# Performance work log

Measured on AMD Instinct MI355X. Metric: run time of the kernel, lower is better.

Reference implementation:

```python
import jax, jax.numpy as jnp
import numpy as np

B, T, E, H = 2, 2048, 2048, 16
D = E // H


def setup_inputs() -> dict:
    key = jax.random.key(0)
    ks = jax.random.split(key, 5)
    s = 0.02
    return {
        "x": jax.random.normal(ks[0], (B, T, E), jnp.float32),
        "Wq": jax.random.normal(ks[1], (E, E), jnp.float32) * s,
        "Wk": jax.random.normal(ks[2], (E, E), jnp.float32) * s,
        "Wv": jax.random.normal(ks[3], (E, E), jnp.float32) * s,
        "Wp": jax.random.normal(ks[4], (E, E), jnp.float32) * s,
        "bp": jnp.zeros((E,), jnp.float32),
    }


def reference(x, Wq, Wk, Wv, Wp, bp):
    b, t, e = x.shape
    h, d = H, E // H
    # torch Linear: y = x @ W.T (no bias for qkv)
    Q = (x @ Wq.T).reshape(b, h, t, d)  # faithful: view without transpose
    K = (x @ Wk.T).reshape(b, h, t, d)
    V = (x @ Wv.T).reshape(b, h, t, d)
    scores = jnp.einsum("bhqd,bhkd->bhqk", Q, K)
    causal = jnp.triu(jnp.ones((t, t), bool), k=1)  # True above diagonal
    scores = jnp.where(causal, -jnp.inf, scores)
    weights = jax.nn.softmax(scores / jnp.sqrt(jnp.float32(d)), axis=-1)
    # dropout p=0.0 (eval) -> identity
    ctx = jnp.einsum("bhqk,bhkd->bhqd", weights, V)  # (b,h,t,d)
    ctx = ctx.transpose(0, 2, 1, 3).reshape(b, t, e)
    return ctx @ Wp.T + bp
```

## Files before the change

### kernel.cpp

```cpp
#include <hip/hip_runtime.h>

#define SEQ   2048
#define EMB   2048
#define NHEAD 16
#define HDIM  128
#define ROWSM 4096

typedef float  f32x4   __attribute__((ext_vector_type(4)));
typedef float  f32x16  __attribute__((ext_vector_type(16)));
typedef __bf16 bf16x8  __attribute__((ext_vector_type(8)));

__device__ __forceinline__ unsigned short f2bf(float f) {
  union { __bf16 b; unsigned short u; } v; v.b = (__bf16)f; return v.u;
}
__device__ __forceinline__ unsigned int pk2(float a, float b) {
  return (unsigned int)f2bf(a) | ((unsigned int)f2bf(b) << 16);
}
__device__ __forceinline__ float max3f(float a, float b, float c) {
  return fmaxf(fmaxf(a, b), c);
}

__device__ __forceinline__ void gload16(const void* g, void* l) {
  __builtin_amdgcn_global_load_lds(
      (__attribute__((address_space(1))) const unsigned int*)g,
      (__attribute__((address_space(3))) unsigned int*)l,
      16, 0, 0);
}

__global__ void cvt_bf16(const float* __restrict__ in,
                         unsigned short* __restrict__ out, int n4) {
  int i = blockIdx.x * 256 + threadIdx.x;
  if (i >= n4) return;
  float4 v = ((const float4*)in)[i];
  ushort4 o;
  o.x = f2bf(v.x); o.y = f2bf(v.y); o.z = f2bf(v.z); o.w = f2bf(v.w);
  ((ushort4*)out)[i] = o;
}

__global__ void cvt_bf16_3(const float* __restrict__ i0, const float* __restrict__ i1,
                           const float* __restrict__ i2, unsigned short* __restrict__ o,
                           int n4) {
  const float* in = (blockIdx.z == 0) ? i0 : (blockIdx.z == 1) ? i1 : i2;
  unsigned short* out = o + (size_t)blockIdx.z * EMB * EMB;
  int i = blockIdx.x * 256 + threadIdx.x;
  if (i >= n4) return;
  float4 v = ((const float4*)in)[i];
  ushort4 o4;
  o4.x = f2bf(v.x); o4.y = f2bf(v.y); o4.z = f2bf(v.z); o4.w = f2bf(v.w);
  ((ushort4*)out)[i] = o4;
}

__global__ __launch_bounds__(512, 1) void gemm192_qkv(
    const unsigned short* __restrict__ A, const unsigned short* __restrict__ B,
    unsigned short* __restrict__ Cb) {
  __shared__ __align__(16) unsigned short At[2][256 * 64];
  __shared__ __align__(16) unsigned short Bt[2][192 * 64];

  const int tid  = threadIdx.x;
  const int lane = tid & 63;
  const int w    = tid >> 6;
  const int wr   = w >> 2;
  const int wc   = w & 3;
  const int lg   = lane >> 4;
  const int lc   = lane & 15;

  const int bid = blockIdx.x;
  const int xcd = bid & 7;
  const int j   = bid >> 3;
  const int mt  = xcd * 2 + (j >> 5);
  const int nt  = j & 31;
  const int m0 = mt * 256;
  const int n0 = nt * 192;

  const int srow8 = lane >> 3;
  const int sslot = (lane & 7) ^ srow8;
  const int NT = EMB / 64;

  auto stageAeven = [&](int ts) {
    if (ts >= NT) return;
    int buf = ts & 1, k0 = ts * 64;
    { int c = w;      int row = c * 8 + srow8;
      gload16(A + (size_t)(m0 + row) * EMB + k0 + sslot * 8, (char*)&At[buf][0] + c * 1024); }
    { int c = 16 + w; int row = c * 8 + srow8;
      gload16(A + (size_t)(m0 + row) * EMB + k0 + sslot * 8, (char*)&At[buf][0] + c * 1024); }
  };
  auto stageAodd = [&](int ts) {
    if (ts >= NT) return;
    int buf = ts & 1, k0 = ts * 64;
    { int c = 8 + w;  int row = c * 8 + srow8;
      gload16(A + (size_t)(m0 + row) * EMB + k0 + sslot * 8, (char*)&At[buf][0] + c * 1024); }
    { int c = 24 + w; int row = c * 8 + srow8;
      gload16(A + (size_t)(m0 + row) * EMB + k0 + sslot * 8, (char*)&At[buf][0] + c * 1024); }
  };
  auto stageB = [&](int ts) {
    if (ts >= NT) return;
    int buf = ts & 1, k0 = ts * 64;
#pragma unroll
    for (int s = 0; s < 3; ++s) {
      int c = w + s * 8;
      int row = c * 8 + srow8;
      gload16(B + (size_t)(n0 + row) * EMB + k0 + sslot * 8, (char*)&Bt[buf][0] + c * 1024);
    }
  };

  f32x4 acc[8][3] = {};
  bf16x8 afr[4][2], bfr[3][2];

  stageAeven(0); stageB(0); stageAodd(0); stageAeven(1); stageB(1);
  asm volatile("s_waitcnt vmcnt(7)" ::: "memory");
  __builtin_amdgcn_s_barrier();

  for (int t = 0; t < NT; ++t) {
    const char* ab = (const char*)&At[t & 1][0];
    const char* bb = (const char*)&Bt[t & 1][0];

#pragma unroll
    for (int ni = 0; ni < 3; ++ni)
#pragma unroll
      for (int kk = 0; kk < 2; ++kk) {
        int row = wc * 48 + ni * 16 + lc;
        bfr[ni][kk] = *(const bf16x8*)(bb + row * 128 + ((((kk << 2) | lg) ^ (lc & 7)) << 4));
      }
#pragma unroll
    for (int mi = 0; mi < 4; ++mi)
#pragma unroll
      for (int kk = 0; kk < 2; ++kk) {
        int row = wr * 128 + mi * 16 + lc;
        afr[mi][kk] = *(const bf16x8*)(ab + row * 128 + ((((kk << 2) | lg) ^ (lc & 7)) << 4));
      }
    stageAodd(t + 1);
    __builtin_amdgcn_s_barrier();
    asm volatile("s_waitcnt lgkmcnt(0)" ::: "memory");
    __builtin_amdgcn_sched_barrier(0);
    __builtin_amdgcn_s_setprio(1);
#pragma unroll
    for (int mi = 0; mi < 4; ++mi)
#pragma unroll
      for (int ni = 0; ni < 3; ++ni)
#pragma unroll
        for (int kk = 0; kk < 2; ++kk)
          acc[mi][ni] = __builtin_amdgcn_mfma_f32_16x16x32_bf16(
              afr[mi][kk], bfr[ni][kk], acc[mi][ni], 0, 0, 0);
    __builtin_amdgcn_s_setprio(0);
    if (t + 1 < NT) asm volatile("s_waitcnt vmcnt(7)" ::: "memory");
    else            asm volatile("s_waitcnt vmcnt(0)" ::: "memory");
    __builtin_amdgcn_s_barrier();

#pragma unroll
    for (int mi = 0; mi < 4; ++mi)
#pragma unroll
      for (int kk = 0; kk < 2; ++kk) {
        int row = wr * 128 + 64 + mi * 16 + lc;
        afr[mi][kk] = *(const bf16x8*)(ab + row * 128 + ((((kk << 2) | lg) ^ (lc & 7)) << 4));
      }
    stageAeven(t + 2); stageB(t + 2);
    __builtin_amdgcn_s_barrier();
    asm volatile("s_waitcnt lgkmcnt(0)" ::: "memory");
    __builtin_amdgcn_sched_barrier(0);
    __builtin_amdgcn_s_setprio(1);
#pragma unroll
    for (int mi = 0; mi < 4; ++mi)
#pragma unroll
      for (int ni = 0; ni < 3; ++ni)
#pragma unroll
        for (int kk = 0; kk < 2; ++kk)
          acc[4 + mi][ni] = __builtin_amdgcn_mfma_f32_16x16x32_bf16(
              afr[mi][kk], bfr[ni][kk], acc[4 + mi][ni], 0, 0, 0);
    __builtin_amdgcn_s_setprio(0);
    if (t + 2 < NT)      asm volatile("s_waitcnt vmcnt(7)" ::: "memory");
    else if (t + 1 < NT) asm volatile("s_waitcnt vmcnt(2)" ::: "memory");
    __builtin_amdgcn_s_barrier();
  }

#pragma unroll
  for (int mi = 0; mi < 8; ++mi)
#pragma unroll
    for (int ni = 0; ni < 3; ++ni) {
      int col = n0 + wc * 48 + ni * 16 + lc;
      unsigned short* dst = Cb + (size_t)(col >> 11) * ROWSM * EMB + (col & 2047);
#pragma unroll
      for (int rr = 0; rr < 4; ++rr) {
        int row = m0 + wr * 128 + mi * 16 + lg * 4 + rr;
        dst[(size_t)row * EMB] = f2bf(acc[mi][ni][rr]);
      }
    }
}

__global__ __launch_bounds__(512, 1) void gemm_p8(
    const unsigned short* __restrict__ A, const unsigned short* __restrict__ B,
    float* __restrict__ Cout, const float* __restrict__ bias) {
  __shared__ __align__(16) unsigned short At[2][128 * 64];
  __shared__ __align__(16) unsigned short Bt[2][256 * 64];

  const int tid  = threadIdx.x;
  const int lane = tid & 63;
  const int w    = tid >> 6;
  const int wr   = w >> 2;
  const int wc   = w & 3;
  const int lg   = lane >> 4;
  const int lc   = lane & 15;

  const int bid = blockIdx.x;
  const int xcd = bid & 7;
  const int j   = bid >> 3;
  const int mt  = xcd * 4 + (j >> 3);
  const int nt  = j & 7;
  const int m0 = mt * 128;
  const int n0 = nt * 256;

  const int srow8 = lane >> 3;
  const int sslot = (lane & 7) ^ srow8;
  const int NT = EMB / 64;

  auto stageA = [&](int ts) {
    if (ts >= NT) return;
    int buf = ts & 1, k0 = ts * 64;
#pragma unroll
    for (int rr = 0; rr < 2; ++rr) {
      int c = w + rr * 8;
      int row = c * 8 + srow8;
      gload16(A + (size_t)(m0 + row) * EMB + k0 + sslot * 8, (char*)&At[buf][0] + c * 1024);
    }
  };
  auto stageBlow = [&](int ts) {
    if (ts >= NT) return;
    int buf = ts & 1, k0 = ts * 64;
#pragma unroll
    for (int rr = 0; rr < 2; ++rr) {
      int i = w + rr * 8;
      int c = (i >> 2) * 8 + (i & 3);
      int row = c * 8 + srow8;
      gload16(B + (size_t)(n0 + row) * EMB + k0 + sslot * 8, (char*)&Bt[buf][0] + c * 1024);
    }
  };
  auto stageBhigh = [&](int ts) {
    if (ts >= NT) return;
    int buf = ts & 1, k0 = ts * 64;
#pragma unroll
    for (int rr = 0; rr < 2; ++rr) {
      int i = w + rr * 8;
      int c = (i >> 2) * 8 + 4 + (i & 3);
      int row = c * 8 + srow8;
      gload16(B + (size_t)(n0 + row) * EMB + k0 + sslot * 8, (char*)&Bt[buf][0] + c * 1024);
    }
  };

  f32x4 acc[4][4] = {};
  bf16x8 afr[4][2], bfr0[2][2], bfr1[2][2];

  stageA(0); stageBlow(0); stageBhigh(0); stageA(1); stageBlow(1);
  asm volatile("s_waitcnt vmcnt(6)" ::: "memory");
  __builtin_amdgcn_s_barrier();

  for (int t = 0; t < NT; ++t) {
    const char* ab = (const char*)&At[t & 1][0];
    const char* bb = (const char*)&Bt[t & 1][0];

#pragma unroll
    for (int ni = 0; ni < 2; ++ni)
#pragma unroll
      for (int kk = 0; kk < 2; ++kk) {
        int row = wc * 64 + ni * 16 + lc;
        bfr0[ni][kk] = *(const bf16x8*)(bb + row * 128 + ((((kk << 2) | lg) ^ (lc & 7)) << 4));
      }
#pragma unroll
    for (int mi = 0; mi < 4; ++mi)
#pragma unroll
      for (int kk = 0; kk < 2; ++kk) {
        int row = wr * 64 + mi * 16 + lc;
        afr[mi][kk] = *(const bf16x8*)(ab + row * 128 + ((((kk << 2) | lg) ^ (lc & 7)) << 4));
      }
    stageBhigh(t + 1);
    __builtin_amdgcn_s_barrier();
    asm volatile("s_waitcnt lgkmcnt(0)" ::: "memory");
    __builtin_amdgcn_sched_barrier(0);
    __builtin_amdgcn_s_setprio(1);
#pragma unroll
    for (int mi = 0; mi < 4; ++mi)
#pragma unroll
      for (int ni = 0; ni < 2; ++ni)
#pragma unroll
        for (int kk = 0; kk < 2; ++kk)
          acc[mi][ni] = __builtin_amdgcn_mfma_f32_16x16x32_bf16(
              afr[mi][kk], bfr0[ni][kk], acc[mi][ni], 0, 0, 0);
    __builtin_amdgcn_s_setprio(0);
    if (t + 1 < NT) asm volatile("s_waitcnt vmcnt(6)" ::: "memory");
    else            asm volatile("s_waitcnt vmcnt(0)" ::: "memory");
    __builtin_amdgcn_s_barrier();

#pragma unroll
    for (int ni = 0; ni < 2; ++ni)
#pragma unroll
      for (int kk = 0; kk < 2; ++kk) {
        int row = wc * 64 + 32 + ni * 16 + lc;
        bfr1[ni][kk] = *(const bf16x8*)(bb + row * 128 + ((((kk << 2) | lg) ^ (lc & 7)) << 4));
      }
    stageA(t + 2); stageBlow(t + 2);
    __builtin_amdgcn_s_barrier();
    asm volatile("s_waitcnt lgkmcnt(0)" ::: "memory");
    __builtin_amdgcn_sched_barrier(0);
    __builtin_amdgcn_s_setprio(1);
#pragma unroll
    for (int mi = 0; mi < 4; ++mi)
#pragma unroll
      for (int ni = 0; ni < 2; ++ni)
#pragma unroll
        for (int kk = 0; kk < 2; ++kk)
          acc[mi][2 + ni] = __builtin_amdgcn_mfma_f32_16x16x32_bf16(
              afr[mi][kk], bfr1[ni][kk], acc[mi][2 + ni], 0, 0, 0);
    __builtin_amdgcn_s_setprio(0);
    if (t + 2 < NT)      asm volatile("s_waitcnt vmcnt(6)" ::: "memory");
    else if (t + 1 < NT) asm volatile("s_waitcnt vmcnt(2)" ::: "memory");
    __builtin_amdgcn_s_barrier();
  }

#pragma unroll
  for (int mi = 0; mi < 4; ++mi)
#pragma unroll
    for (int ni = 0; ni < 4; ++ni) {
      int col = n0 + wc * 64 + ((ni >> 1) * 32) + (ni & 1) * 16 + lc;
#pragma unroll
      for (int rr = 0; rr < 4; ++rr) {
        int row = m0 + wr * 64 + mi * 16 + lg * 4 + rr;
        Cout[(size_t)row * EMB + col] = acc[mi][ni][rr] + bias[col];
      }
    }
}

__global__ __launch_bounds__(256, 2) void attn_causal(
    const unsigned short* __restrict__ Pq, const unsigned short* __restrict__ Pk,
    const unsigned short* __restrict__ Pv, unsigned short* __restrict__ ctx) {
  __shared__ __align__(16) unsigned short Ks[128 * 128];
  __shared__ __align__(16) unsigned short Vt[128 * 128];

  const int tid  = threadIdx.x;
  const int lane = tid & 63;
  const int w    = tid >> 6;
  const int ql   = lane & 31;
  const int hi   = lane >> 5;
  const int lg   = lane >> 4;
  const int lc   = lane & 15;

  const int bid = blockIdx.x;
  const int xcd = bid & 7;
  const int jj_ = bid >> 3;
  const int hh  = jj_ >> 4;
  const int bh  = xcd * 4 + hh;
  const int b   = bh >> 4;
  const int h   = bh & 15;
  const int qtr = jj_ & 15;
  const int qt  = (hh >= 2) ? (15 - qtr) : qtr;
  const int q0 = qt * 128;
  const int qw = q0 + w * 32;
  const int qg = qw + ql;

  const size_t hoff = (size_t)bh * SEQ * HDIM;
  const unsigned short* Q  = Pq + hoff;
  const unsigned short* Kh = Pk + hoff;
  const unsigned short* Vh = Pv + hoff;

  bf16x8 bq[8];
#pragma unroll
  for (int d8 = 0; d8 < 8; ++d8)
    bq[d8] = *(const bf16x8*)(Q + (size_t)qg * HDIM + d8 * 16 + hi * 8);

  const float NEG = -3.0e38f;
  f32x16 o[4];
#pragma unroll
  for (int dt = 0; dt < 4; ++dt)
#pragma unroll
    for (int r = 0; r < 16; ++r) o[dt][r] = 0.f;
  float m_r = NEG, l_r = 0.f;

  const float Cs   = 0.12753123161692858f;
  const float TDEF = 62.7f;

  const int nt128 = qt + 1;
  for (int tt = 0; tt < nt128; ++tt) {
    const int kv0 = tt * 128;
    if (tt) __syncthreads();
#pragma unroll
    for (int ii = 0; ii < 8; ++ii) {
      int i = w * 8 + ii;
      int r = i * 4 + lg;
      int sd = lc ^ (r & 7);
      gload16(Kh + (size_t)(kv0 + r) * HDIM + sd * 8, (char*)Ks + i * 1024);
    }
#pragma unroll 1
    for (int hv = 0; hv < 2; ++hv) {
      uint4 vr[4];
      const unsigned short* Vs = Vh + (size_t)(kv0 + hv * 64) * HDIM;
#pragma unroll
      for (int uu = 0; uu < 2; ++uu) {
        int u = tid + uu * 256;
        int kp = u >> 4, dg = u & 15;
        int k = kp * 2, d0 = dg * 8;
        vr[uu * 2]     = *(const uint4*)(Vs + (size_t)k * HDIM + d0);
        vr[uu * 2 + 1] = *(const uint4*)(Vs + (size_t)(k + 1) * HDIM + d0);
      }
#pragma unroll
      for (int uu = 0; uu < 2; ++uu) {
        int u = tid + uu * 256;
        int kp = u >> 4, dg = u & 15;
        int k = kp * 2, d0 = dg * 8;
        const unsigned short* e0 = (const unsigned short*)&vr[uu * 2];
        const unsigned short* e1 = (const unsigned short*)&vr[uu * 2 + 1];
#pragma unroll
        for (int jj = 0; jj < 8; ++jj) {
          int d = d0 + jj;
          int slot = ((hv << 3) | (k >> 3)) ^ jj ^ (dg & 7);
          int byteoff = d * 256 + (slot << 4) + (k & 7) * 2;
          *(unsigned int*)((char*)Vt + byteoff) =
              (unsigned int)e0[jj] | ((unsigned int)e1[jj] << 16);
        }
      }
    }
    __syncthreads();

#pragma unroll 1
    for (int hf = 0; hf < 2; ++hf) {
      const int kv0h = kv0 + hf * 64;
      if (kv0h > qw + 31) continue;
      const bool s1on = (kv0h + 32 <= qw + 31);
      const bool diag = (kv0h + 63 > qw);
      const char* ksb = (const char*)Ks + hf * 64 * 256;

      f32x16 c0, c1;
#pragma unroll
      for (int r = 0; r < 16; ++r) { c0[r] = 0.f; c1[r] = s1on ? 0.f : NEG; }
      __builtin_amdgcn_s_setprio(1);
#pragma unroll
      for (int d8 = 0; d8 < 8; ++d8) {
        bf16x8 ak = *(const bf16x8*)(ksb + ql * 256 +
                                     (((d8 * 2 + hi) ^ (ql & 7)) << 4));
        c0 = __builtin_amdgcn_mfma_f32_32x32x16_bf16(ak, bq[d8], c0, 0, 0, 0);
      }
      if (s1on) {
#pragma unroll
        for (int d8 = 0; d8 < 8; ++d8) {
          bf16x8 ak = *(const bf16x8*)(ksb + (32 + ql) * 256 +
                                       (((d8 * 2 + hi) ^ (ql & 7)) << 4));
          c1 = __builtin_amdgcn_mfma_f32_32x32x16_bf16(ak, bq[d8], c1, 0, 0, 0);
        }
      }
      __builtin_amdgcn_s_setprio(0);

      if (diag) {
#pragma unroll
        for (int r = 0; r < 16; ++r) {
          int kvl = (r & 3) + 8 * (r >> 2) + 4 * hi;
          if (kv0h + kvl > qg) c0[r] = NEG;
          if (s1on && kv0h + 32 + kvl > qg) c1[r] = NEG;
        }
      }
      float rm;
      {
        float a0 = max3f(c0[0],  c0[1],  c0[2]);
        float a1 = max3f(c0[3],  c0[4],  c0[5]);
        float a2 = max3f(c0[6],  c0[7],  c0[8]);
        float a3 = max3f(c0[9],  c0[10], c0[11]);
        float a4 = max3f(c0[12], c0[13], c0[14]);
        float a5 = max3f(c0[15], c1[0],  c1[1]);
        float a6 = max3f(c1[2],  c1[3],  c1[4]);
        float a7 = max3f(c1[5],  c1[6],  c1[7]);
        float a8 = max3f(c1[8],  c1[9],  c1[10]);
        float a9 = max3f(c1[11], c1[12], c1[13]);
        float aa = fmaxf(c1[14], c1[15]);
        float b0 = max3f(a0, a1, a2);
        float b1 = max3f(a3, a4, a5);
        float b2 = max3f(a6, a7, a8);
        float b3 = max3f(a9, aa, NEG);
        rm = fmaxf(fmaxf(b0, b1), fmaxf(b2, b3));
      }
      rm = fmaxf(rm, __shfl_xor(rm, 32));

      if (__any(rm > m_r + TDEF)) {
        float mnew = fmaxf(m_r, rm);
        float alpha = exp2f((m_r - mnew) * Cs);
        m_r = mnew;
        l_r *= alpha;
#pragma unroll
        for (int r = 0; r < 16; ++r) {
          float ar = __shfl(alpha, (r & 3) + 8 * (r >> 2) + 4 * hi);
#pragma unroll
          for (int dt = 0; dt < 4; ++dt) o[dt][r] *= ar;
        }
      }
#pragma unroll
      for (int r = 0; r < 16; ++r) {
        c0[r] = exp2f((c0[r] - m_r) * Cs);
        c1[r] = exp2f((c1[r] - m_r) * Cs);
      }
      float ps = 0.f;
#pragma unroll
      for (int r = 0; r < 16; ++r) ps += c0[r] + c1[r];
      ps += __shfl_xor(ps, 32);
      l_r += ps;

      bf16x8 pa[4];
#pragma unroll
      for (int t4 = 0; t4 < 4; ++t4) {
        const f32x16& cc = (t4 < 2) ? c0 : c1;
        const int rA = (t4 & 1) * 8;
        unsigned int pkL0 = pk2(cc[rA + 0], cc[rA + 1]);
        unsigned int pkL1 = pk2(cc[rA + 2], cc[rA + 3]);
        unsigned int pkH0 = pk2(cc[rA + 4], cc[rA + 5]);
        unsigned int pkH1 = pk2(cc[rA + 6], cc[rA + 7]);
        unsigned int give0 = hi ? pkL0 : pkH0;
        unsigned int give1 = hi ? pkL1 : pkH1;
        unsigned int keep0 = hi ? pkH0 : pkL0;
        unsigned int keep1 = hi ? pkH1 : pkL1;
        unsigned int recv0 = __shfl_xor(give0, 32);
        unsigned int recv1 = __shfl_xor(give1, 32);
        union { unsigned int u[4]; bf16x8 v; } pu;
        pu.u[0] = hi ? recv0 : keep0;
        pu.u[1] = hi ? recv1 : keep1;
        pu.u[2] = hi ? keep0 : recv0;
        pu.u[3] = hi ? keep1 : recv1;
        pa[t4] = pu.v;
      }
      __builtin_amdgcn_s_setprio(1);
#pragma unroll
      for (int t4 = 0; t4 < 4; ++t4) {
        if (diag && kv0h + t4 * 16 > qw + 31) continue;
#pragma unroll
        for (int dt = 0; dt < 4; ++dt) {
          int d = dt * 32 + ql;
          int slot = ((hf << 3) | (t4 << 1) | hi) ^ (d & 7) ^ ((d >> 3) & 7);
          bf16x8 bv = *(const bf16x8*)((const char*)Vt + d * 256 + (slot << 4));
          o[dt] = __builtin_amdgcn_mfma_f32_32x32x16_bf16(pa[t4], bv, o[dt], 0, 0, 0);
        }
      }
      __builtin_amdgcn_s_setprio(0);
    }
  }

  float linv = 1.0f / l_r;
  unsigned short* outp = ctx + (size_t)b * SEQ * EMB + (size_t)h * HDIM;
#pragma unroll
  for (int r = 0; r < 16; ++r) {
    int kvl = (r & 3) + 8 * (r >> 2) + 4 * hi;
    float lr = __shfl(linv, kvl);
    int qrow = qw + kvl;
#pragma unroll
    for (int dt = 0; dt < 4; ++dt)
      outp[(size_t)qrow * EMB + dt * 32 + ql] = f2bf(o[dt][r] * lr);
  }
}

extern "C" void kernel_launch(void* const* d_in, const int* in_sizes, int n_in,
                              void* d_out, int out_size, void* d_ws, size_t ws_size,
                              hipStream_t stream) {
  const float* x  = (const float*)d_in[0];
  const float* Wq = (const float*)d_in[1];
  const float* Wk = (const float*)d_in[2];
  const float* Wv = (const float*)d_in[3];
  const float* Wp = (const float*)d_in[4];
  const float* bp = (const float*)d_in[5];

  char* ws = (char*)d_ws;
  unsigned short* xb = (unsigned short*)ws;
  unsigned short* Wb = (unsigned short*)(ws + (size_t)(16u << 20));
  unsigned short* Pq = (unsigned short*)(ws + (size_t)(24u << 20));
  unsigned short* Pk = (unsigned short*)(ws + (size_t)(40u << 20));
  unsigned short* Pv = (unsigned short*)(ws + (size_t)(56u << 20));
  unsigned short* WB3 = (unsigned short*)d_out;

  const int nX4 = ROWSM * EMB / 4;
  const int nW4 = EMB * EMB / 4;

  cvt_bf16<<<nX4 / 256, 256, 0, stream>>>(x, xb, nX4);
  cvt_bf16_3<<<dim3(nW4 / 256, 1, 3), 256, 0, stream>>>(Wq, Wk, Wv, WB3, nW4);

  gemm192_qkv<<<512, 512, 0, stream>>>(xb, WB3, Pq);

  attn_causal<<<512, 256, 0, stream>>>(Pq, Pk, Pv, xb);

  cvt_bf16<<<nW4 / 256, 256, 0, stream>>>(Wp, Wb, nW4);
  gemm_p8<<<256, 512, 0, stream>>>(xb, Wb, (float*)d_out, bp);
}
```

Measured before the change: 256.9 us.

## Double-buffer 64-row K/V tiles in attention and merge all conversions

The causal attention kernel now works on 64-row KV tiles in double-buffered LDS. K for tile t+2 is prefetched asynchronously and V for the next tile is held in registers, with explicit waitcnt and barrier calls so loads overlap the MFMA work instead of stalling at each 128-row tile. Separately, the four fp32-to-bf16 conversion launches (x, Wq/Wk/Wv, Wp) are merged into one launch with a z dimension of 5, removing two kernel launches. The hand-written vmcnt counts are fragile and depend on how the compiler orders memory operations. The merged conversion also launches many idle blocks for the smaller weight slices.

```diff
diff --git a/kernel.cpp b/kernel.cpp
--- a/kernel.cpp
+++ b/kernel.cpp
@@ -27,21 +27,20 @@
       16, 0, 0);
 }
 
-__global__ void cvt_bf16(const float* __restrict__ in,
-                         unsigned short* __restrict__ out, int n4) {
-  int i = blockIdx.x * 256 + threadIdx.x;
-  if (i >= n4) return;
-  float4 v = ((const float4*)in)[i];
-  ushort4 o;
-  o.x = f2bf(v.x); o.y = f2bf(v.y); o.z = f2bf(v.z); o.w = f2bf(v.w);
-  ((ushort4*)out)[i] = o;
-}
-
-__global__ void cvt_bf16_3(const float* __restrict__ i0, const float* __restrict__ i1,
-                           const float* __restrict__ i2, unsigned short* __restrict__ o,
-                           int n4) {
-  const float* in = (blockIdx.z == 0) ? i0 : (blockIdx.z == 1) ? i1 : i2;
-  unsigned short* out = o + (size_t)blockIdx.z * EMB * EMB;
+__global__ void cvt_all(const float* __restrict__ x,  const float* __restrict__ Wq,
+                        const float* __restrict__ Wk, const float* __restrict__ Wv,
+                        const float* __restrict__ Wp, unsigned short* __restrict__ xb,
+                        unsigned short* __restrict__ WB3, unsigned short* __restrict__ Wb,
+                        int nX4, int nW4) {
+  const int z = blockIdx.z;
+  const float* in;
+  unsigned short* out;
+  int n4;
+  if (z == 0)      { in = x;  out = xb;  n4 = nX4; }
+  else if (z == 1) { in = Wq; out = WB3;                          n4 = nW4; }
+  else if (z == 2) { in = Wk; out = WB3 + (size_t)EMB * EMB;      n4 = nW4; }
+  else if (z == 3) { in = Wv; out = WB3 + (size_t)2 * EMB * EMB;  n4 = nW4; }
+  else             { in = Wp; out = Wb;  n4 = nW4; }
   int i = blockIdx.x * 256 + threadIdx.x;
   if (i >= n4) return;
   float4 v = ((const float4*)in)[i];
@@ -330,8 +329,8 @@
 __global__ __launch_bounds__(256, 2) void attn_causal(
     const unsigned short* __restrict__ Pq, const unsigned short* __restrict__ Pk,
     const unsigned short* __restrict__ Pv, unsigned short* __restrict__ ctx) {
-  __shared__ __align__(16) unsigned short Ks[128 * 128];
-  __shared__ __align__(16) unsigned short Vt[128 * 128];
+  __shared__ __align__(16) unsigned short Ks[2][64 * 128];
+  __shared__ __align__(16) unsigned short Vt[2][128 * 64];
 
   const int tid  = threadIdx.x;
   const int lane = tid & 63;
@@ -375,55 +374,74 @@
   const float Cs   = 0.12753123161692858f;
   const float TDEF = 62.7f;
 
-  const int nt128 = qt + 1;
-  for (int tt = 0; tt < nt128; ++tt) {
-    const int kv0 = tt * 128;
-    if (tt) __syncthreads();
-#pragma unroll
-    for (int ii = 0; ii < 8; ++ii) {
-      int i = w * 8 + ii;
+  auto stageK = [&](int buf, int t) {
+    int kv0 = t * 64;
+#pragma unroll
+    for (int ii = 0; ii < 4; ++ii) {
+      int i = w * 4 + ii;
       int r = i * 4 + lg;
       int sd = lc ^ (r & 7);
-      gload16(Kh + (size_t)(kv0 + r) * HDIM + sd * 8, (char*)Ks + i * 1024);
-    }
-#pragma unroll 1
-    for (int hv = 0; hv < 2; ++hv) {
-      uint4 vr[4];
-      const unsigned short* Vs = Vh + (size_t)(kv0 + hv * 64) * HDIM;
-#pragma unroll
-      for (int uu = 0; uu < 2; ++uu) {
-        int u = tid + uu * 256;
-        int kp = u >> 4, dg = u & 15;
-        int k = kp * 2, d0 = dg * 8;
-        vr[uu * 2]     = *(const uint4*)(Vs + (size_t)k * HDIM + d0);
-        vr[uu * 2 + 1] = *(const uint4*)(Vs + (size_t)(k + 1) * HDIM + d0);
-      }
-#pragma unroll
-      for (int uu = 0; uu < 2; ++uu) {
-        int u = tid + uu * 256;
-        int kp = u >> 4, dg = u & 15;
-        int k = kp * 2, d0 = dg * 8;
-        const unsigned short* e0 = (const unsigned short*)&vr[uu * 2];
-        const unsigned short* e1 = (const unsigned short*)&vr[uu * 2 + 1];
-#pragma unroll
-        for (int jj = 0; jj < 8; ++jj) {
-          int d = d0 + jj;
-          int slot = ((hv << 3) | (k >> 3)) ^ jj ^ (dg & 7);
-          int byteoff = d * 256 + (slot << 4) + (k & 7) * 2;
-          *(unsigned int*)((char*)Vt + byteoff) =
-              (unsigned int)e0[jj] | ((unsigned int)e1[jj] << 16);
-        }
-      }
-    }
-    __syncthreads();
-
-#pragma unroll 1
-    for (int hf = 0; hf < 2; ++hf) {
-      const int kv0h = kv0 + hf * 64;
-      if (kv0h > qw + 31) continue;
-      const bool s1on = (kv0h + 32 <= qw + 31);
-      const bool diag = (kv0h + 63 > qw);
-      const char* ksb = (const char*)Ks + hf * 64 * 256;
+      gload16(Kh + (size_t)(kv0 + r) * HDIM + sd * 8, (char*)&Ks[buf][0] + i * 1024);
+    }
+  };
+  auto loadV = [&](uint4* vr, int t) {
+    int kv0 = t * 64;
+#pragma unroll
+    for (int uu = 0; uu < 2; ++uu) {
+      int u = tid + uu * 256;
+      int kp = u >> 4, dg = u & 15;
+      int k = kp * 2, d0 = dg * 8;
+      vr[uu * 2]     = *(const uint4*)(Vh + (size_t)(kv0 + k) * HDIM + d0);
+      vr[uu * 2 + 1] = *(const uint4*)(Vh + (size_t)(kv0 + k + 1) * HDIM + d0);
+    }
+  };
+  auto packV = [&](int buf, const uint4* vr) {
+#pragma unroll
+    for (int uu = 0; uu < 2; ++uu) {
+      int u = tid + uu * 256;
+      int kp = u >> 4, dg = u & 15;
+      int k = kp * 2, d0 = dg * 8;
+      const unsigned short* e0 = (const unsigned short*)&vr[uu * 2];
+      const unsigned short* e1 = (const unsigned short*)&vr[uu * 2 + 1];
+#pragma unroll
+      for (int jj = 0; jj < 8; ++jj) {
+        int d = d0 + jj;
+        int slot = (k >> 3) ^ jj ^ (dg & 7);
+        int byteoff = d * 128 + (slot << 4) + (k & 7) * 2;
+        *(unsigned int*)((char*)&Vt[buf][0] + byteoff) =
+            (unsigned int)e0[jj] | ((unsigned int)e1[jj] << 16);
+      }
+    }
+  };
+
+  const int ntiles = 2 * qt + 2;
+  uint4 vr[4];
+
+  loadV(vr, 0); stageK(0, 0);
+  asm volatile("s_waitcnt vmcnt(4)" ::: "memory");
+  packV(0, vr);
+  loadV(vr, 1); stageK(1, 1);
+  asm volatile("s_waitcnt vmcnt(8)" ::: "memory");
+  asm volatile("s_waitcnt lgkmcnt(0)" ::: "memory");
+  __builtin_amdgcn_s_barrier();
+
+  for (int t = 0; t < ntiles; ++t) {
+    const int buf = t & 1;
+    const bool hasN1 = (t + 1 < ntiles);
+    const bool hasN2 = (t + 2 < ntiles);
+    const int kv0 = t * 64;
+
+    if (hasN1) {
+      asm volatile("s_waitcnt vmcnt(4)" ::: "memory");
+      packV(buf ^ 1, vr);
+      if (hasN2) loadV(vr, t + 2);
+    }
+
+    if (kv0 <= qw + 31) {
+      const bool s1on = (kv0 + 32 <= qw + 31);
+      const bool diag = (kv0 + 63 > qw);
+      const char* ksb = (const char*)&Ks[buf][0];
+      const char* vtb = (const char*)&Vt[buf][0];
 
       f32x16 c0, c1;
 #pragma unroll
@@ -449,8 +467,8 @@
 #pragma unroll
         for (int r = 0; r < 16; ++r) {
           int kvl = (r & 3) + 8 * (r >> 2) + 4 * hi;
-          if (kv0h + kvl > qg) c0[r] = NEG;
-          if (s1on && kv0h + 32 + kvl > qg) c1[r] = NEG;
+          if (kv0 + kvl > qg) c0[r] = NEG;
+          if (s1on && kv0 + 32 + kvl > qg) c1[r] = NEG;
         }
       }
       float rm;
@@ -522,17 +540,25 @@
       __builtin_amdgcn_s_setprio(1);
 #pragma unroll
       for (int t4 = 0; t4 < 4; ++t4) {
-        if (diag && kv0h + t4 * 16 > qw + 31) continue;
+        if (diag && kv0 + t4 * 16 > qw + 31) continue;
 #pragma unroll
         for (int dt = 0; dt < 4; ++dt) {
           int d = dt * 32 + ql;
-          int slot = ((hf << 3) | (t4 << 1) | hi) ^ (d & 7) ^ ((d >> 3) & 7);
-          bf16x8 bv = *(const bf16x8*)((const char*)Vt + d * 256 + (slot << 4));
+          int slot = ((t4 << 1) | hi) ^ (d & 7) ^ ((d >> 3) & 7);
+          bf16x8 bv = *(const bf16x8*)(vtb + d * 128 + (slot << 4));
           o[dt] = __builtin_amdgcn_mfma_f32_32x32x16_bf16(pa[t4], bv, o[dt], 0, 0, 0);
         }
       }
       __builtin_amdgcn_s_setprio(0);
     }
+
+    if (hasN2) stageK(buf, t + 2);
+    asm volatile("s_waitcnt lgkmcnt(0)" ::: "memory");
+    if (hasN1) {
+      if (hasN2) asm volatile("s_waitcnt vmcnt(8)" ::: "memory");
+      else       asm volatile("s_waitcnt vmcnt(0)" ::: "memory");
+    }
+    __builtin_amdgcn_s_barrier();
   }
 
   float linv = 1.0f / l_r;
@@ -569,13 +595,12 @@
   const int nX4 = ROWSM * EMB / 4;
   const int nW4 = EMB * EMB / 4;
 
-  cvt_bf16<<<nX4 / 256, 256, 0, stream>>>(x, xb, nX4);
-  cvt_bf16_3<<<dim3(nW4 / 256, 1, 3), 256, 0, stream>>>(Wq, Wk, Wv, WB3, nW4);
+  cvt_all<<<dim3(nX4 / 256, 1, 5), 256, 0, stream>>>(
+      x, Wq, Wk, Wv, Wp, xb, WB3, Wb, nX4, nW4);
 
   gemm192_qkv<<<512, 512, 0, stream>>>(xb, WB3, Pq);
 
   attn_causal<<<512, 256, 0, stream>>>(Pq, Pk, Pv, xb);
 
-  cvt_bf16<<<nW4 / 256, 256, 0, stream>>>(Wp, Wb, nW4);
   gemm_p8<<<256, 512, 0, stream>>>(xb, Wb, (float*)d_out, bp);
 }
```

Measured after the change: 257.0 us, median of 4. About the same (+0.1%).
